# Optimization experiments

Measured on AMD Instinct MI355X. Metric: run time of the kernel, lower is better.

Reference implementation:

```python
import jax, jax.numpy as jnp
import numpy as np

K_CHUNK = 512  # key-chunk size used by the module when n > 5000


def setup_inputs() -> dict:
    key = jax.random.key(0)
    ks = jax.random.split(key, 9)
    b, n, d = 1, 8192, 512
    s = 1.0 / np.sqrt(d)
    x = jax.random.normal(ks[0], (b, n, d), dtype=jnp.float32)
    Wq = jax.random.normal(ks[1], (d, d), dtype=jnp.float32) * s
    bq = jax.random.normal(ks[2], (d,), dtype=jnp.float32) * 0.01
    Wk = jax.random.normal(ks[3], (d, d), dtype=jnp.float32) * s
    bk = jax.random.normal(ks[4], (d,), dtype=jnp.float32) * 0.01
    Wv = jax.random.normal(ks[5], (d, d), dtype=jnp.float32) * s
    bv = jax.random.normal(ks[6], (d,), dtype=jnp.float32) * 0.01
    Wo = jax.random.normal(ks[7], (d, d), dtype=jnp.float32) * s
    bo = jax.random.normal(ks[8], (d,), dtype=jnp.float32) * 0.01
    return {"x": x, "Wq": Wq, "bq": bq, "Wk": Wk, "bk": bk,
            "Wv": Wv, "bv": bv, "Wo": Wo, "bo": bo}


def reference(x, Wq, bq, Wk, bk, Wv, bv, Wo, bo):
    # Faithful to the n > 5000 branch of SimpleAttenLayer (eval mode: dropout = identity).
    # The q-chunking in the original does not change the math (each q row is independent),
    # so we vectorize over all queries. The k-chunking DOES change the math: softmax is
    # applied within each 512-wide key block, then a second softmax over the concatenated
    # per-block weights, then matmul with full v.
    b, n, d = x.shape
    assert n % K_CHUNK == 0
    q = x @ Wq + bq
    k = x @ Wk + bk
    v = x @ Wv + bv
    scores = jnp.einsum('bnd,bmd->bnm', q, k) / jnp.sqrt(jnp.float32(d))
    # softmax within each key chunk of size K_CHUNK
    w1 = jax.nn.softmax(scores.reshape(b, n, n // K_CHUNK, K_CHUNK), axis=-1)
    w1 = w1.reshape(b, n, n)
    # second (global) softmax over the concatenated chunk weights
    w2 = jax.nn.softmax(w1, axis=-1)
    attn_out = jnp.einsum('bnm,bmd->bnd', w2, v)
    cls_attn_weights = w2[:, 0:1, :]  # [b, 1, n]
    out = x + (attn_out @ Wo + bo)
    return (out, cls_attn_weights)
```

## Files before the change

kernel.cpp:

```cpp
#include <hip/hip_runtime.h>
#include <stdint.h>

typedef unsigned short u16;
typedef uint8_t u8;
typedef __bf16 bf16x8 __attribute__((ext_vector_type(8)));
typedef float f32x4 __attribute__((ext_vector_type(4)));
typedef long i64x2 __attribute__((ext_vector_type(2)));

#define NTOK 8192
#define DD 512
#define CHK 512
#define NCH 16
#define KSPLIT 4
#define KLEN 2048
#define LOG2E 1.4426950408889634f
#define SCL 0.044194173824159216f
#define SCLL 0.063762069130835270f

__device__ __forceinline__ u16 f2bf(float f) {
  union { float f; uint32_t u; } v; v.f = f;
  uint32_t r = v.u + 0x7FFFu + ((v.u >> 16) & 1u);
  return (u16)(r >> 16);
}

template <int CTRL>
__device__ __forceinline__ float dppadd(float x) {
  int y = __builtin_amdgcn_update_dpp(0, __float_as_int(x), CTRL, 0xF, 0xF, true);
  return x + __int_as_float(y);
}
__device__ __forceinline__ float rowsum16(float x) {
  x = dppadd<0xB1>(x);
  x = dppadd<0x4E>(x);
  x = dppadd<0x141>(x);
  x = dppadd<0x140>(x);
  return x;
}

typedef const __attribute__((address_space(1))) unsigned int* gas_t;
typedef __attribute__((address_space(3))) unsigned int* las_t;
__device__ __forceinline__ void gload16(const void* g, void* l) {
  __builtin_amdgcn_global_load_lds((gas_t)g, (las_t)l, 16, 0, 0);
}

__device__ __forceinline__ int ilv64(int p) {
  const int g = p >> 3;
  return (((g & 3) * 2) + (g >> 2)) * 8 + (p & 7);
}
__device__ __forceinline__ int fperm(int t) {
  const int p = ((t & 15) << 2) | ((t >> 4) & 3);
  return (t & ~63) | ilv64(p);
}

__global__ void prep_kernel(const float* __restrict__ x, const float* __restrict__ Wq,
                            const float* __restrict__ Wk, const float* __restrict__ Wv,
                            const float* __restrict__ Wo, const float* __restrict__ bq,
                            u16* __restrict__ xb, u16* __restrict__ Wall, u16* __restrict__ WoT,
                            float* __restrict__ lsum, float* __restrict__ q0g) {
  __shared__ float t[32][33];
  const int bid = blockIdx.x;
  const int tid = threadIdx.x;
  if (bid < 4096) {
    int i = bid * 256 + tid;
    if (bid < 32) lsum[bid * 256 + tid] = 0.f;
    float4 v = ((const float4*)x)[i];
    ushort4 o;
    o.x = f2bf(v.x); o.y = f2bf(v.y); o.z = f2bf(v.z); o.w = f2bf(v.w);
    ((ushort4*)xb)[i] = o;
  } else if (bid < 5120) {
    const int tt = bid - 4096;
    const int z = tt >> 8, idx = tt & 255;
    const float* W; u16* WT;
    if (z == 0)      { W = Wq; WT = Wall; }
    else if (z == 1) { W = Wk; WT = Wall + 512 * 512; }
    else if (z == 2) { W = Wv; WT = Wall + 2 * 512 * 512; }
    else             { W = Wo; WT = WoT; }
    const int n0 = (idx & 15) * 32, k0 = (idx >> 4) * 32;
    const int tx = tid & 31, ty = tid >> 5;
    #pragma unroll
    for (int i = 0; i < 4; i++)
      t[ty + 8 * i][tx] = W[(k0 + ty + 8 * i) * DD + n0 + tx];
    __syncthreads();
    #pragma unroll
    for (int i = 0; i < 4; i++)
      WT[(n0 + ty + 8 * i) * DD + k0 + tx] = f2bf(t[tx][ty + 8 * i]);
  } else {
    const int c = (bid - 5120) * 256 + tid;
    float acc = bq[c];
    #pragma unroll 8
    for (int i = 0; i < 512; i++) acc += x[i] * Wq[i * 512 + c];
    q0g[c] = acc;
  }
}

__launch_bounds__(256, 3)
__global__ void qkv_kernel(const u16* __restrict__ A, const u16* __restrict__ Wall,
                           const float* __restrict__ bq, const float* __restrict__ bk,
                           const float* __restrict__ bv, u8* __restrict__ qb8,
                           u8* __restrict__ kb8, u8* __restrict__ vT8) {
  __shared__ __align__(16) u16 As[128 * 32];
  __shared__ __align__(16) u16 Bs[128 * 32];
  const int m0 = blockIdx.x * 128;
  const int n0g = blockIdx.y * 128;
  const int which = blockIdx.y >> 2;
  const int n0 = n0g & 511;
  const int tid = threadIdx.x;
  const int w = tid >> 6, lane = tid & 63, lm = lane & 15, quad = lane >> 4;
  const int wm = w & 1, wn = w >> 1;
  f32x4 acc[4][4] = {};
  const int soff = tid * 16;
  const int srow = soff >> 6;
  const int scol = soff & 63;
  const char* Ag = (const char*)A + ((size_t)(m0 + srow) * DD) * 2 + scol;
  const char* Bg = (const char*)Wall + ((size_t)(n0g + srow) * DD) * 2 + scol;
  char* Al = (char*)As + w * 1024;
  char* Bl = (char*)Bs + w * 1024;
  const size_t rs = (size_t)64 * DD * 2;
  for (int kk = 0; kk < DD; kk += 32) {
    const char* ag = Ag + (size_t)kk * 2;
    const char* bg = Bg + (size_t)kk * 2;
    gload16(ag, Al);
    gload16(ag + rs, Al + 4096);
    gload16(bg, Bl);
    gload16(bg + rs, Bl + 4096);
    __syncthreads();
    bf16x8 af[4], bfr[4];
    #pragma unroll
    for (int i = 0; i < 4; i++) af[i] = *(const bf16x8*)&As[(wm * 64 + i * 16 + lm) * 32 + quad * 8];
    #pragma unroll
    for (int j = 0; j < 4; j++) bfr[j] = *(const bf16x8*)&Bs[(wn * 64 + j * 16 + lm) * 32 + quad * 8];
    #pragma unroll
    for (int i = 0; i < 4; i++)
      #pragma unroll
      for (int j = 0; j < 4; j++)
        acc[i][j] = __builtin_amdgcn_mfma_f32_16x16x32_bf16(af[i], bfr[j], acc[i][j], 0, 0, 0);
    __syncthreads();
  }
  const float* bias = (which == 0) ? bq : (which == 1) ? bk : bv;
  #pragma unroll
  for (int i = 0; i < 4; i++) {
    const int row0 = m0 + wm * 64 + i * 16 + quad * 4;
    #pragma unroll
    for (int j = 0; j < 4; j++) {
      const int col = n0 + wn * 64 + j * 16 + lm;
      const float bv_ = bias[col];
      if (which == 2) {
        #pragma unroll
        for (int r = 0; r < 4; r++) {
          const float val = acc[i][j][r] + bv_;
          uint32_t pk = __builtin_amdgcn_cvt_pk_fp8_f32(val, val, 0, false);
          vT8[(size_t)col * NTOK + fperm(row0 + r)] = (u8)(pk & 0xFF);
        }
      } else {
        u8* dst = (which == 0) ? qb8 : kb8;
        const int icol = (col & ~63) | ilv64(col & 63);
        #pragma unroll
        for (int r = 0; r < 4; r++) {
          const float val = acc[i][j][r] + bv_;
          uint32_t pk = __builtin_amdgcn_cvt_pk_fp8_f32(val, val, 0, false);
          dst[(size_t)(row0 + r) * DD + icol] = (u8)(pk & 0xFF);
        }
      }
    }
  }
}

__launch_bounds__(256, 3)
__global__ void outproj_kernel(const u16* __restrict__ A, const u16* __restrict__ BT,
                               const float* __restrict__ bias, float* __restrict__ outp,
                               const float* __restrict__ resid) {
  __shared__ __align__(16) u16 As[128 * 32];
  __shared__ __align__(16) u16 Bs[128 * 32];
  const int m0 = blockIdx.x * 128, n0 = blockIdx.y * 128;
  const int tid = threadIdx.x;
  const int w = tid >> 6, lane = tid & 63, lm = lane & 15, quad = lane >> 4;
  const int wm = w & 1, wn = w >> 1;
  f32x4 acc[4][4] = {};
  const int soff = tid * 16;
  const int srow = soff >> 6;
  const int scol = soff & 63;
  const char* Ag = (const char*)A + ((size_t)(m0 + srow) * DD) * 2 + scol;
  const char* Bg = (const char*)BT + ((size_t)(n0 + srow) * DD) * 2 + scol;
  char* Al = (char*)As + w * 1024;
  char* Bl = (char*)Bs + w * 1024;
  const size_t rs = (size_t)64 * DD * 2;
  for (int kk = 0; kk < DD; kk += 32) {
    const char* ag = Ag + (size_t)kk * 2;
    const char* bg = Bg + (size_t)kk * 2;
    gload16(ag, Al);
    gload16(ag + rs, Al + 4096);
    gload16(bg, Bl);
    gload16(bg + rs, Bl + 4096);
    __syncthreads();
    bf16x8 af[4], bfr[4];
    #pragma unroll
    for (int i = 0; i < 4; i++) af[i] = *(const bf16x8*)&As[(wm * 64 + i * 16 + lm) * 32 + quad * 8];
    #pragma unroll
    for (int j = 0; j < 4; j++) bfr[j] = *(const bf16x8*)&Bs[(wn * 64 + j * 16 + lm) * 32 + quad * 8];
    #pragma unroll
    for (int i = 0; i < 4; i++)
      #pragma unroll
      for (int j = 0; j < 4; j++)
        acc[i][j] = __builtin_amdgcn_mfma_f32_16x16x32_bf16(af[i], bfr[j], acc[i][j], 0, 0, 0);
    __syncthreads();
  }
  #pragma unroll
  for (int i = 0; i < 4; i++) {
    const int row0 = m0 + wm * 64 + i * 16 + quad * 4;
    #pragma unroll
    for (int j = 0; j < 4; j++) {
      const int col = n0 + wn * 64 + j * 16 + lm;
      const float bv = bias[col];
      #pragma unroll
      for (int r = 0; r < 4; r++) {
        const size_t idx = (size_t)(row0 + r) * DD + col;
        outp[idx] = acc[i][j][r] + bv + resid[idx];
      }
    }
  }
}

template <int MODE>
__launch_bounds__(256, 3)
__global__ void gemm_fp8_kernel(const u8* __restrict__ A, const u8* __restrict__ BT,
                                int K, int lda, int ldb, void* __restrict__ outp,
                                const float* __restrict__ lsum) {
  __shared__ __align__(16) u8 As[128 * 64];
  __shared__ __align__(16) u8 Bs[128 * 64];
  const int m0 = blockIdx.x * 128, n0 = blockIdx.y * 128;
  const int tid = threadIdx.x;
  const int w = tid >> 6, lane = tid & 63, lm = lane & 15, quad = lane >> 4;
  const int wm = w & 1, wn = w >> 1;
  f32x4 acc[4][4] = {};
  const int srow = tid >> 2;
  const int scol = ((tid & 3) ^ ((srow >> 1) & 3)) * 16;
  const size_t kbase = (MODE == 4) ? (size_t)blockIdx.z * (size_t)K : 0;
  const u8* Ag = A + (size_t)(m0 + srow) * lda + kbase + scol;
  const u8* Bg = BT + (size_t)(n0 + srow) * ldb + kbase + scol;
  u8* Al = As + w * 1024;
  u8* Bl = Bs + w * 1024;
  const size_t ars = (size_t)64 * lda;
  const size_t brs = (size_t)64 * ldb;
  const int csel = ((quad ^ ((lm >> 1) & 3)) * 16);
  for (int kk = 0; kk < K; kk += 64) {
    const u8* ag = Ag + kk;
    const u8* bg = Bg + kk;
    gload16(ag, Al);
    gload16(ag + ars, Al + 4096);
    gload16(bg, Bl);
    gload16(bg + brs, Bl + 4096);
    __syncthreads();
    i64x2 afv[4], bfv[4];
    #pragma unroll
    for (int i = 0; i < 4; i++)
      afv[i] = *(const i64x2*)&As[(wm * 64 + i * 16 + lm) * 64 + csel];
    #pragma unroll
    for (int j = 0; j < 4; j++)
      bfv[j] = *(const i64x2*)&Bs[(wn * 64 + j * 16 + lm) * 64 + csel];
    #pragma unroll
    for (int i = 0; i < 4; i++)
      #pragma unroll
      for (int j = 0; j < 4; j++) {
        acc[i][j] = __builtin_amdgcn_mfma_f32_16x16x32_fp8_fp8(afv[i].x, bfv[j].x, acc[i][j], 0, 0, 0);
        acc[i][j] = __builtin_amdgcn_mfma_f32_16x16x32_fp8_fp8(afv[i].y, bfv[j].y, acc[i][j], 0, 0, 0);
      }
    __syncthreads();
  }
  #pragma unroll
  for (int i = 0; i < 4; i++) {
    const int row0 = m0 + wm * 64 + i * 16 + quad * 4;
    float li[4];
    if (MODE == 3) {
      #pragma unroll
      for (int r = 0; r < 4; r++) li[r] = 1.0f / lsum[row0 + r];
    }
    #pragma unroll
    for (int j = 0; j < 4; j++) {
      const int col = n0 + wn * 64 + j * 16 + lm;
      if (MODE == 3) {
        #pragma unroll
        for (int r = 0; r < 4; r++)
          ((u16*)outp)[(size_t)(row0 + r) * DD + col] = f2bf(acc[i][j][r] * li[r]);
      } else {
        float* po = (float*)outp + (size_t)blockIdx.z * NTOK * DD;
        #pragma unroll
        for (int r = 0; r < 4; r++)
          po[(size_t)(row0 + r) * DD + col] = acc[i][j][r];
      }
    }
  }
}

__global__ void pv_reduce_kernel(const float* __restrict__ part, const float* __restrict__ lsum,
                                 u16* __restrict__ attnb) {
  const int idx = blockIdx.x * 256 + threadIdx.x;
  const int row = idx >> 7;
  const int c4 = (idx & 127) << 2;
  const float* p = part + (size_t)row * DD + c4;
  const size_t stride = (size_t)NTOK * DD;
  float4 a = *(const float4*)(p);
  float4 b = *(const float4*)(p + stride);
  float4 c = *(const float4*)(p + 2 * stride);
  float4 d = *(const float4*)(p + 3 * stride);
  const float inv = 1.0f / lsum[row];
  ushort4 o;
  o.x = f2bf((a.x + b.x + c.x + d.x) * inv);
  o.y = f2bf((a.y + b.y + c.y + d.y) * inv);
  o.z = f2bf((a.z + b.z + c.z + d.z) * inv);
  o.w = f2bf((a.w + b.w + c.w + d.w) * inv);
  *(ushort4*)(attnb + (size_t)row * DD + c4) = o;
}

__launch_bounds__(512, 4)
__global__ void scores_kernel(const u8* __restrict__ qb8, const u8* __restrict__ kb8,
                              u8* __restrict__ P8, float* __restrict__ lsum) {
  __shared__ __align__(16) u8 As[64 * 64];
  __shared__ __align__(16) u8 Bs[512 * 64];
  __shared__ float hS[8][64], hP[8][64], hZ[64];
  const int m0 = blockIdx.x * 64;
  const int c = blockIdx.y;
  const int tid = threadIdx.x;
  const int w = tid >> 6, lane = tid & 63, lm = lane & 15, quad = lane >> 4;
  const int wsl = w;
  f32x4 s[4][4] = {};
  const int srA = tid >> 2;
  const int scS = ((tid & 3) ^ ((srA >> 1) & 3)) * 16;
  const u8* Qg = qb8 + (size_t)(m0 + srA) * DD + scS;
  const u8* Kg = kb8 + (size_t)(c * CHK + srA) * DD + scS;
  u8* Al = As + w * 1024;
  u8* Bl = Bs + w * 1024;
  const int csel = ((quad ^ ((lm >> 1) & 3)) * 16);
  for (int kk = 0; kk < DD; kk += 64) {
    if (tid < 256) gload16(Qg + kk, Al);
    gload16(Kg + kk, Bl);
    gload16(Kg + kk + (size_t)128 * DD, Bl + 8192);
    gload16(Kg + kk + (size_t)256 * DD, Bl + 16384);
    gload16(Kg + kk + (size_t)384 * DD, Bl + 24576);
    __syncthreads();
    i64x2 afv[4], bfv[4];
    #pragma unroll
    for (int i = 0; i < 4; i++)
      afv[i] = *(const i64x2*)&As[(i * 16 + lm) * 64 + csel];
    #pragma unroll
    for (int j = 0; j < 4; j++)
      bfv[j] = *(const i64x2*)&Bs[(wsl * 64 + j * 16 + lm) * 64 + csel];
    #pragma unroll
    for (int i = 0; i < 4; i++)
      #pragma unroll
      for (int j = 0; j < 4; j++) {
        s[i][j] = __builtin_amdgcn_mfma_f32_16x16x32_fp8_fp8(afv[i].x, bfv[j].x, s[i][j], 0, 0, 0);
        s[i][j] = __builtin_amdgcn_mfma_f32_16x16x32_fp8_fp8(afv[i].y, bfv[j].y, s[i][j], 0, 0, 0);
      }
    __syncthreads();
  }
  #pragma unroll
  for (int i = 0; i < 4; i++) {
    #pragma unroll
    for (int reg = 0; reg < 4; reg++) {
      float z = 0.f;
      #pragma unroll
      for (int j = 0; j < 4; j++) {
        float e = exp2f(s[i][j][reg] * SCLL);
        s[i][j][reg] = e;
        z += e;
      }
      z = rowsum16(z);
      if (lm == 0) hS[wsl][i * 16 + quad * 4 + reg] = z;
    }
  }
  __syncthreads();
  if (tid < 64) {
    float t = 0.f;
    #pragma unroll
    for (int w2 = 0; w2 < 8; w2++) t += hS[w2][tid];
    hZ[tid] = LOG2E / t;
  }
  __syncthreads();
  const int newc = ((lm >> 1) & 3) * 2 + (lm >> 3);
  const int pbyte = wsl * 64 + newc * 8 + (lm & 1) * 4;
  #pragma unroll
  for (int i = 0; i < 4; i++) {
    #pragma unroll
    for (int reg = 0; reg < 4; reg++) {
      const int rl = i * 16 + quad * 4 + reg;
      const float iz = hZ[rl];
      const float p0 = exp2f(s[i][0][reg] * iz);
      const float p1 = exp2f(s[i][1][reg] * iz);
      const float p2 = exp2f(s[i][2][reg] * iz);
      const float p3 = exp2f(s[i][3][reg] * iz);
      float zp = (p0 + p1) + (p2 + p3);
      zp = rowsum16(zp);
      if (lm == 0) hP[wsl][rl] = zp;
      uint32_t o = __builtin_amdgcn_cvt_pk_fp8_f32(p0, p1, 0, false);
      o = __builtin_amdgcn_cvt_pk_fp8_f32(p2, p3, o, true);
      *(uint32_t*)(P8 + (size_t)(m0 + rl) * NTOK + c * CHK + pbyte) = o;
    }
  }
  __syncthreads();
  if (tid < 64) {
    float t = 0.f;
    #pragma unroll
    for (int w2 = 0; w2 < 8; w2++) t += hP[w2][tid];
    atomicAdd(&lsum[m0 + tid], t);
  }
}

__global__ void cls_u_kernel(const float* __restrict__ Wk, const float* __restrict__ bk,
                             const float* __restrict__ q0g, float* __restrict__ uc) {
  __shared__ float q0[512];
  const int tid = threadIdx.x;
  q0[tid] = q0g[tid];
  q0[tid + 256] = q0g[tid + 256];
  __syncthreads();
  if (blockIdx.x < 8) {
    const int c = blockIdx.x * 64 + (tid >> 2), ii = tid & 3;
    float acc = 0.f;
    #pragma unroll 8
    for (int j = ii; j < 512; j += 4) acc += Wk[(size_t)c * 512 + j] * q0[j];
    acc += __shfl_xor(acc, 1, 64);
    acc += __shfl_xor(acc, 2, 64);
    if (ii == 0) uc[c] = acc;
  } else if (tid < 64) {
    float acc = 0.f;
    #pragma unroll 8
    for (int j = tid; j < 512; j += 64) acc += bk[j] * q0[j];
    #pragma unroll
    for (int off = 1; off < 64; off <<= 1) acc += __shfl_xor(acc, off, 64);
    if (tid == 0) uc[512] = acc;
  }
}

__global__ void cls_scores_kernel(const float* __restrict__ x, const float* __restrict__ uc,
                                  float* __restrict__ s0) {
  __shared__ float u[512];
  __shared__ float c0s;
  int tid = threadIdx.x;
  for (int i = tid; i < 512; i += 256) u[i] = uc[i];
  if (tid == 0) c0s = uc[512];
  __syncthreads();
  int rowg = blockIdx.x * 32 + (tid >> 3);
  int ii = tid & 7;
  const float* xr = x + rowg * 512;
  float acc = 0.f;
  for (int i = ii; i < 512; i += 8) acc += xr[i] * u[i];
  acc += __shfl_xor(acc, 1, 64);
  acc += __shfl_xor(acc, 2, 64);
  acc += __shfl_xor(acc, 4, 64);
  if (ii == 0) s0[rowg] = (acc + c0s) * SCL;
}

__global__ void cls_softmax_kernel(const float* __restrict__ s0, float* __restrict__ out) {
  int tid = threadIdx.x;
  int w = tid >> 6, lane = tid & 63;
  const float* sc = s0 + w * 512;
  float v[8];
  float m = -1e30f;
  #pragma unroll
  for (int j = 0; j < 8; j++) { v[j] = sc[lane * 8 + j]; m = fmaxf(m, v[j]); }
  for (int off = 1; off < 64; off <<= 1) m = fmaxf(m, __shfl_xor(m, off, 64));
  float z = 0.f;
  #pragma unroll
  for (int j = 0; j < 8; j++) { v[j] = expf(v[j] - m); z += v[j]; }
  for (int off = 1; off < 64; off <<= 1) z += __shfl_xor(z, off, 64);
  float invz = 1.f / z;
  float l = 0.f;
  #pragma unroll
  for (int j = 0; j < 8; j++) { v[j] = expf(v[j] * invz); l += v[j]; }
  for (int off = 1; off < 64; off <<= 1) l += __shfl_xor(l, off, 64);
  __shared__ float lw[16];
  if (lane == 0) lw[w] = l;
  __syncthreads();
  float L = 0.f;
  for (int i = 0; i < 16; i++) L += lw[i];
  float invL = 1.f / L;
  #pragma unroll
  for (int j = 0; j < 8; j++) out[w * 512 + lane * 8 + j] = v[j] * invL;
}

extern "C" void kernel_launch(void* const* d_in, const int* in_sizes, int n_in,
                              void* d_out, int out_size, void* d_ws, size_t ws_size,
                              hipStream_t stream) {
  const float* x  = (const float*)d_in[0];
  const float* Wq = (const float*)d_in[1];
  const float* bq = (const float*)d_in[2];
  const float* Wk = (const float*)d_in[3];
  const float* bk = (const float*)d_in[4];
  const float* Wv = (const float*)d_in[5];
  const float* bv = (const float*)d_in[6];
  const float* Wo = (const float*)d_in[7];
  const float* bo = (const float*)d_in[8];
  float* out = (float*)d_out;

  char* ws = (char*)d_ws;
  u16* xb    = (u16*)(ws);
  u16* Wall  = (u16*)(ws + 8388608);
  u16* WoT   = (u16*)(ws + 9961472);
  u8*  qb8   = (u8*)(ws + 10485760);
  u8*  kb8   = (u8*)(ws + 14680064);
  u8*  vT8   = (u8*)(ws + 18874368);
  u16* attnb = (u16*)(ws + 23068672);
  float* q0g = (float*)(ws + 31457280);
  float* uc  = (float*)(ws + 31461376);
  float* s0  = (float*)(ws + 31465472);
  float* lsum= (float*)(ws + 31498240);
  u8*  P8    = (u8*)(ws + 31531008);
  float* part= (float*)(ws + 98639872);
  const size_t need_full = 98639872ULL + (size_t)KSPLIT * NTOK * DD * 4ULL;

  prep_kernel<<<5122, 256, 0, stream>>>(x, Wq, Wk, Wv, Wo, bq, xb, Wall, WoT, lsum, q0g);

  qkv_kernel<<<dim3(NTOK / 128, 12), 256, 0, stream>>>(xb, Wall, bq, bk, bv, qb8, kb8, vT8);

  scores_kernel<<<dim3(NTOK / 64, NCH), 512, 0, stream>>>(qb8, kb8, P8, lsum);

  if (ws_size >= need_full) {
    gemm_fp8_kernel<4><<<dim3(NTOK / 128, DD / 128, KSPLIT), 256, 0, stream>>>(
        P8, vT8, KLEN, NTOK, NTOK, part, nullptr);
    pv_reduce_kernel<<<NTOK * DD / 4 / 256, 256, 0, stream>>>(part, lsum, attnb);
  } else {
    gemm_fp8_kernel<3><<<dim3(NTOK / 128, DD / 128), 256, 0, stream>>>(
        P8, vT8, NTOK, NTOK, NTOK, attnb, lsum);
  }

  outproj_kernel<<<dim3(NTOK / 128, DD / 128), 256, 0, stream>>>(attnb, WoT, bo, out, x);

  cls_u_kernel<<<9, 256, 0, stream>>>(Wk, bk, q0g, uc);
  cls_scores_kernel<<<NTOK / 32, 256, 0, stream>>>(x, uc, s0);
  cls_softmax_kernel<<<1, 1024, 0, stream>>>(s0, out + (size_t)NTOK * DD);
}
```

Before: 304.0 us.

## Double-buffer LDS tiles in GEMM and scores kernels to overlap loads with MFMA

The qkv, outproj, fp8 GEMM and scores kernels now keep two LDS buffers per operand. Each iteration issues the global-to-LDS loads for the next K slice before running the MFMAs on the current one, so memory latency can overlap compute. Each iteration ends with a single explicit vmcnt(0) wait plus barrier instead of two __syncthreads, and the scores kernel raises wave priority around its MFMA block. The cost is double the shared memory: in the scores kernel it grows to roughly 72KB per block, which may cut resident blocks per CU and hurt occupancy.

Result: no change. 302.1 us (-0.6%).

```diff
diff --git a/kernel.cpp b/kernel.cpp
--- a/kernel.cpp
+++ b/kernel.cpp
@@ -40,6 +40,14 @@
 typedef __attribute__((address_space(3))) unsigned int* las_t;
 __device__ __forceinline__ void gload16(const void* g, void* l) {
   __builtin_amdgcn_global_load_lds((gas_t)g, (las_t)l, 16, 0, 0);
+}
+
+__device__ __forceinline__ void vm0bar() {
+  asm volatile("s_waitcnt vmcnt(0)\n\ts_barrier" ::: "memory");
+}
+__device__ __forceinline__ void lgkm0() {
+  asm volatile("s_waitcnt lgkmcnt(0)" ::: "memory");
+  __builtin_amdgcn_sched_barrier(0);
 }
 
 __device__ __forceinline__ int ilv64(int p) {
@@ -97,8 +105,8 @@
                            const float* __restrict__ bq, const float* __restrict__ bk,
                            const float* __restrict__ bv, u8* __restrict__ qb8,
                            u8* __restrict__ kb8, u8* __restrict__ vT8) {
-  __shared__ __align__(16) u16 As[128 * 32];
-  __shared__ __align__(16) u16 Bs[128 * 32];
+  __shared__ __align__(16) u16 As[2][128 * 32];
+  __shared__ __align__(16) u16 Bs[2][128 * 32];
   const int m0 = blockIdx.x * 128;
   const int n0g = blockIdx.y * 128;
   const int which = blockIdx.y >> 2;
@@ -115,25 +123,35 @@
   char* Al = (char*)As + w * 1024;
   char* Bl = (char*)Bs + w * 1024;
   const size_t rs = (size_t)64 * DD * 2;
-  for (int kk = 0; kk < DD; kk += 32) {
+
+  auto stage = [&](int kk, int buf) {
     const char* ag = Ag + (size_t)kk * 2;
     const char* bg = Bg + (size_t)kk * 2;
-    gload16(ag, Al);
-    gload16(ag + rs, Al + 4096);
-    gload16(bg, Bl);
-    gload16(bg + rs, Bl + 4096);
-    __syncthreads();
+    char* al = Al + buf * 8192;
+    char* bl = Bl + buf * 8192;
+    gload16(ag, al);
+    gload16(ag + rs, al + 4096);
+    gload16(bg, bl);
+    gload16(bg + rs, bl + 4096);
+  };
+
+  stage(0, 0);
+  vm0bar();
+  for (int t = 0; t < 16; ++t) {
+    const int cur = t & 1;
+    if (t < 15) stage((t + 1) * 32, cur ^ 1);
     bf16x8 af[4], bfr[4];
     #pragma unroll
-    for (int i = 0; i < 4; i++) af[i] = *(const bf16x8*)&As[(wm * 64 + i * 16 + lm) * 32 + quad * 8];
-    #pragma unroll
-    for (int j = 0; j < 4; j++) bfr[j] = *(const bf16x8*)&Bs[(wn * 64 + j * 16 + lm) * 32 + quad * 8];
+    for (int i = 0; i < 4; i++) af[i] = *(const bf16x8*)&As[cur][(wm * 64 + i * 16 + lm) * 32 + quad * 8];
+    #pragma unroll
+    for (int j = 0; j < 4; j++) bfr[j] = *(const bf16x8*)&Bs[cur][(wn * 64 + j * 16 + lm) * 32 + quad * 8];
+    lgkm0();
     #pragma unroll
     for (int i = 0; i < 4; i++)
       #pragma unroll
       for (int j = 0; j < 4; j++)
         acc[i][j] = __builtin_amdgcn_mfma_f32_16x16x32_bf16(af[i], bfr[j], acc[i][j], 0, 0, 0);
-    __syncthreads();
+    vm0bar();
   }
   const float* bias = (which == 0) ? bq : (which == 1) ? bk : bv;
   #pragma unroll
@@ -168,8 +186,8 @@
 __global__ void outproj_kernel(const u16* __restrict__ A, const u16* __restrict__ BT,
                                const float* __restrict__ bias, float* __restrict__ outp,
                                const float* __restrict__ resid) {
-  __shared__ __align__(16) u16 As[128 * 32];
-  __shared__ __align__(16) u16 Bs[128 * 32];
+  __shared__ __align__(16) u16 As[2][128 * 32];
+  __shared__ __align__(16) u16 Bs[2][128 * 32];
   const int m0 = blockIdx.x * 128, n0 = blockIdx.y * 128;
   const int tid = threadIdx.x;
   const int w = tid >> 6, lane = tid & 63, lm = lane & 15, quad = lane >> 4;
@@ -183,25 +201,35 @@
   char* Al = (char*)As + w * 1024;
   char* Bl = (char*)Bs + w * 1024;
   const size_t rs = (size_t)64 * DD * 2;
-  for (int kk = 0; kk < DD; kk += 32) {
+
+  auto stage = [&](int kk, int buf) {
     const char* ag = Ag + (size_t)kk * 2;
     const char* bg = Bg + (size_t)kk * 2;
-    gload16(ag, Al);
-    gload16(ag + rs, Al + 4096);
-    gload16(bg, Bl);
-    gload16(bg + rs, Bl + 4096);
-    __syncthreads();
+    char* al = Al + buf * 8192;
+    char* bl = Bl + buf * 8192;
+    gload16(ag, al);
+    gload16(ag + rs, al + 4096);
+    gload16(bg, bl);
+    gload16(bg + rs, bl + 4096);
+  };
+
+  stage(0, 0);
+  vm0bar();
+  for (int t = 0; t < 16; ++t) {
+    const int cur = t & 1;
+    if (t < 15) stage((t + 1) * 32, cur ^ 1);
     bf16x8 af[4], bfr[4];
     #pragma unroll
-    for (int i = 0; i < 4; i++) af[i] = *(const bf16x8*)&As[(wm * 64 + i * 16 + lm) * 32 + quad * 8];
-    #pragma unroll
-    for (int j = 0; j < 4; j++) bfr[j] = *(const bf16x8*)&Bs[(wn * 64 + j * 16 + lm) * 32 + quad * 8];
+    for (int i = 0; i < 4; i++) af[i] = *(const bf16x8*)&As[cur][(wm * 64 + i * 16 + lm) * 32 + quad * 8];
+    #pragma unroll
+    for (int j = 0; j < 4; j++) bfr[j] = *(const bf16x8*)&Bs[cur][(wn * 64 + j * 16 + lm) * 32 + quad * 8];
+    lgkm0();
     #pragma unroll
     for (int i = 0; i < 4; i++)
       #pragma unroll
       for (int j = 0; j < 4; j++)
         acc[i][j] = __builtin_amdgcn_mfma_f32_16x16x32_bf16(af[i], bfr[j], acc[i][j], 0, 0, 0);
-    __syncthreads();
+    vm0bar();
   }
   #pragma unroll
   for (int i = 0; i < 4; i++) {
@@ -224,8 +252,8 @@
 __global__ void gemm_fp8_kernel(const u8* __restrict__ A, const u8* __restrict__ BT,
                                 int K, int lda, int ldb, void* __restrict__ outp,
                                 const float* __restrict__ lsum) {
-  __shared__ __align__(16) u8 As[128 * 64];
-  __shared__ __align__(16) u8 Bs[128 * 64];
+  __shared__ __align__(16) u8 As[2][128 * 64];
+  __shared__ __align__(16) u8 Bs[2][128 * 64];
   const int m0 = blockIdx.x * 128, n0 = blockIdx.y * 128;
   const int tid = threadIdx.x;
   const int w = tid >> 6, lane = tid & 63, lm = lane & 15, quad = lane >> 4;
@@ -236,26 +264,36 @@
   const size_t kbase = (MODE == 4) ? (size_t)blockIdx.z * (size_t)K : 0;
   const u8* Ag = A + (size_t)(m0 + srow) * lda + kbase + scol;
   const u8* Bg = BT + (size_t)(n0 + srow) * ldb + kbase + scol;
-  u8* Al = As + w * 1024;
-  u8* Bl = Bs + w * 1024;
+  u8* Al = (u8*)As + w * 1024;
+  u8* Bl = (u8*)Bs + w * 1024;
   const size_t ars = (size_t)64 * lda;
   const size_t brs = (size_t)64 * ldb;
   const int csel = ((quad ^ ((lm >> 1) & 3)) * 16);
-  for (int kk = 0; kk < K; kk += 64) {
+
+  auto stage = [&](int kk, int buf) {
     const u8* ag = Ag + kk;
     const u8* bg = Bg + kk;
-    gload16(ag, Al);
-    gload16(ag + ars, Al + 4096);
-    gload16(bg, Bl);
-    gload16(bg + brs, Bl + 4096);
-    __syncthreads();
+    u8* al = Al + buf * 8192;
+    u8* bl = Bl + buf * 8192;
+    gload16(ag, al);
+    gload16(ag + ars, al + 4096);
+    gload16(bg, bl);
+    gload16(bg + brs, bl + 4096);
+  };
+
+  stage(0, 0);
+  vm0bar();
+  int cur = 0;
+  for (int kk = 0; kk < K; kk += 64) {
+    if (kk + 64 < K) stage(kk + 64, cur ^ 1);
     i64x2 afv[4], bfv[4];
     #pragma unroll
     for (int i = 0; i < 4; i++)
-      afv[i] = *(const i64x2*)&As[(wm * 64 + i * 16 + lm) * 64 + csel];
+      afv[i] = *(const i64x2*)&As[cur][(wm * 64 + i * 16 + lm) * 64 + csel];
     #pragma unroll
     for (int j = 0; j < 4; j++)
-      bfv[j] = *(const i64x2*)&Bs[(wn * 64 + j * 16 + lm) * 64 + csel];
+      bfv[j] = *(const i64x2*)&Bs[cur][(wn * 64 + j * 16 + lm) * 64 + csel];
+    lgkm0();
     #pragma unroll
     for (int i = 0; i < 4; i++)
       #pragma unroll
@@ -263,7 +301,8 @@
         acc[i][j] = __builtin_amdgcn_mfma_f32_16x16x32_fp8_fp8(afv[i].x, bfv[j].x, acc[i][j], 0, 0, 0);
         acc[i][j] = __builtin_amdgcn_mfma_f32_16x16x32_fp8_fp8(afv[i].y, bfv[j].y, acc[i][j], 0, 0, 0);
       }
-    __syncthreads();
+    vm0bar();
+    cur ^= 1;
   }
   #pragma unroll
   for (int i = 0; i < 4; i++) {
@@ -313,8 +352,8 @@
 __launch_bounds__(512, 4)
 __global__ void scores_kernel(const u8* __restrict__ qb8, const u8* __restrict__ kb8,
                               u8* __restrict__ P8, float* __restrict__ lsum) {
-  __shared__ __align__(16) u8 As[64 * 64];
-  __shared__ __align__(16) u8 Bs[512 * 64];
+  __shared__ __align__(16) u8 As[2][64 * 64];
+  __shared__ __align__(16) u8 Bs[2][512 * 64];
   __shared__ float hS[8][64], hP[8][64], hZ[64];
   const int m0 = blockIdx.x * 64;
   const int c = blockIdx.y;
@@ -326,23 +365,35 @@
   const int scS = ((tid & 3) ^ ((srA >> 1) & 3)) * 16;
   const u8* Qg = qb8 + (size_t)(m0 + srA) * DD + scS;
   const u8* Kg = kb8 + (size_t)(c * CHK + srA) * DD + scS;
-  u8* Al = As + w * 1024;
-  u8* Bl = Bs + w * 1024;
+  u8* Al = (u8*)As + w * 1024;
+  u8* Bl = (u8*)Bs + w * 1024;
   const int csel = ((quad ^ ((lm >> 1) & 3)) * 16);
-  for (int kk = 0; kk < DD; kk += 64) {
-    if (tid < 256) gload16(Qg + kk, Al);
-    gload16(Kg + kk, Bl);
-    gload16(Kg + kk + (size_t)128 * DD, Bl + 8192);
-    gload16(Kg + kk + (size_t)256 * DD, Bl + 16384);
-    gload16(Kg + kk + (size_t)384 * DD, Bl + 24576);
-    __syncthreads();
+
+  auto stage = [&](int kk, int buf) {
+    u8* al = Al + buf * 4096;
+    u8* bl = Bl + buf * 32768;
+    if (tid < 256) gload16(Qg + kk, al);
+    gload16(Kg + kk, bl);
+    gload16(Kg + kk + (size_t)128 * DD, bl + 8192);
+    gload16(Kg + kk + (size_t)256 * DD, bl + 16384);
+    gload16(Kg + kk + (size_t)384 * DD, bl + 24576);
+  };
+
+  stage(0, 0);
+  vm0bar();
+  #pragma unroll
+  for (int t = 0; t < 8; ++t) {
+    const int cur = t & 1;
+    if (t < 7) stage((t + 1) * 64, cur ^ 1);
     i64x2 afv[4], bfv[4];
     #pragma unroll
     for (int i = 0; i < 4; i++)
-      afv[i] = *(const i64x2*)&As[(i * 16 + lm) * 64 + csel];
+      afv[i] = *(const i64x2*)&As[cur][(i * 16 + lm) * 64 + csel];
     #pragma unroll
     for (int j = 0; j < 4; j++)
-      bfv[j] = *(const i64x2*)&Bs[(wsl * 64 + j * 16 + lm) * 64 + csel];
+      bfv[j] = *(const i64x2*)&Bs[cur][(wsl * 64 + j * 16 + lm) * 64 + csel];
+    lgkm0();
+    __builtin_amdgcn_s_setprio(1);
     #pragma unroll
     for (int i = 0; i < 4; i++)
       #pragma unroll
@@ -350,7 +401,8 @@
         s[i][j] = __builtin_amdgcn_mfma_f32_16x16x32_fp8_fp8(afv[i].x, bfv[j].x, s[i][j], 0, 0, 0);
         s[i][j] = __builtin_amdgcn_mfma_f32_16x16x32_fp8_fp8(afv[i].y, bfv[j].y, s[i][j], 0, 0, 0);
       }
-    __syncthreads();
+    __builtin_amdgcn_s_setprio(0);
+    vm0bar();
   }
   #pragma unroll
   for (int i = 0; i < 4; i++) {
```
